# Performance work log

Hardware: AMD Instinct MI355X
Metric: run time of the kernel (lower is better)

Reference implementation:

```python
import jax, jax.numpy as jnp
import numpy as np

N = 200000
H = 128        # n_heads == input feature dim
HID = 512      # hidden_features
D_H = 512      # scaling denominator
C = 10.0       # tanh clip scale


def setup_inputs() -> dict:
    key = jax.random.key(0)
    k0, k1, k2, k3, k4, k5 = jax.random.split(key, 6)
    output = jax.random.normal(k0, (N, H), dtype=jnp.float32)
    # adjacency row: binary mask (which nodes are reachable neighbors)
    adj_modified = (jax.random.uniform(k1, (N,)) < 0.5).astype(jnp.float32)
    W1 = jax.random.normal(k2, (HID, H), dtype=jnp.float32) * (1.0 / np.sqrt(H))
    b1 = jax.random.normal(k3, (HID,), dtype=jnp.float32) * 0.01
    W2 = jax.random.normal(k4, (HID, H), dtype=jnp.float32) * (1.0 / np.sqrt(H))
    b2 = jax.random.normal(k5, (HID,), dtype=jnp.float32) * 0.01
    return {"output": output, "adj_modified": adj_modified,
            "W1": W1, "b1": b1, "W2": W2, "b2": b2, "prev_node": 5}


def reference(output, adj_modified, W1, b1, W2, b2, prev_node):
    # v_i: [1, H] embedding of the previously selected node
    v_i = output[prev_node][None, :]
    # v_j: [N, H] neighbor embeddings gated by the adjacency row
    v_j = adj_modified[:, None] * output
    phi1_v_i = v_i @ W1.T + b1          # [1, HID]
    phi2_v_j = v_j @ W2.T + b2          # [N, HID]
    scores = (phi1_v_i @ phi2_v_j.T) / jnp.sqrt(jnp.asarray(D_H, jnp.float32))  # [1, N]
    attn = C * jnp.tanh(scores) * adj_modified  # clipped + masked, [1, N]
    attn = attn[0]                                # [N]
    w = jax.nn.softmax(attn, axis=0)
    w = w * (attn != 0).astype(w.dtype)
    p = w.max()
    selected_node = jnp.argmax(w)
    return selected_node, p
```

## Files before the change

kernel.cpp:

```cpp
#include <hip/hip_runtime.h>
#include <math.h>

#define H 128
#define HID 512
#define GRID 2048
#define PREP_B 16

struct Ws {
    float sb_part[PREP_B];
    float u_part[PREP_B][H];
    unsigned long long best_part[GRID];
    float Z_part[GRID];
};

__device__ __forceinline__ unsigned int fkey(float f) {
    unsigned int u = __float_as_uint(f);
    return (u & 0x80000000u) ? ~u : (u | 0x80000000u);
}
__device__ __forceinline__ float inv_fkey(unsigned int k) {
    return __uint_as_float((k & 0x80000000u) ? (k ^ 0x80000000u) : ~k);
}

__global__ __launch_bounds__(256)
void prep_kernel(const float* __restrict__ outp, const float* __restrict__ W1,
                 const float* __restrict__ b1, const float* __restrict__ W2,
                 const float* __restrict__ b2, const int* __restrict__ prev,
                 Ws* __restrict__ ws) {
    __shared__ float phi1_s[32];
    __shared__ float sb_s[8];
    __shared__ float u_s[2][H];
    int t = threadIdx.x;
    int lane = t & 63;
    int c = lane & 31;
    int g = t >> 5;
    int kbase = blockIdx.x * 32;
    const float4* vi = (const float4*)(outp + (size_t)prev[0] * H);
    float4 v = vi[c];
    float sb = 0.f;
#pragma unroll
    for (int r = 0; r < 4; ++r) {
        int kl = g * 4 + r;
        int k = kbase + kl;
        float4 w = ((const float4*)(W1 + (size_t)k * H))[c];
        float d = w.x * v.x + w.y * v.y + w.z * v.z + w.w * v.w;
        d += __shfl_xor(d, 16);
        d += __shfl_xor(d, 8);
        d += __shfl_xor(d, 4);
        d += __shfl_xor(d, 2);
        d += __shfl_xor(d, 1);
        if (c == 0) {
            float phi = d + b1[k];
            phi1_s[kl] = phi;
            sb += phi * b2[k];
        }
    }
    if (c == 0) sb_s[g] = sb;
    __syncthreads();
    int h = t & 127;
    int g2 = t >> 7;
    float up = 0.f;
#pragma unroll
    for (int kk = 0; kk < 16; ++kk) {
        int kl = g2 * 16 + kk;
        up += phi1_s[kl] * W2[(size_t)(kbase + kl) * H + h];
    }
    u_s[g2][h] = up;
    __syncthreads();
    if (t < H) ws->u_part[blockIdx.x][t] = u_s[0][t] + u_s[1][t];
    if (t == 0) {
        float s = 0.f;
#pragma unroll
        for (int i = 0; i < 8; ++i) s += sb_s[i];
        ws->sb_part[blockIdx.x] = s;
    }
}

__global__ __launch_bounds__(256)
void score_kernel(const float4* __restrict__ xv, const float* __restrict__ adj,
                  Ws* __restrict__ ws, int n, int ntiles) {
    __shared__ float zs[4];
    __shared__ unsigned long long bs[4];
    const float inv = 0.04419417382415922f;
    int t = threadIdx.x;
    int lane = t & 63;
    int c = lane & 31;
    int hv = lane >> 5;
    int w = t >> 6;
    float4 uv = make_float4(0.f, 0.f, 0.f, 0.f);
    float s_b = 0.f;
#pragma unroll
    for (int b = 0; b < PREP_B; ++b) {
        float4 p = ((const float4*)ws->u_part[b])[c];
        uv.x += p.x; uv.y += p.y; uv.z += p.z; uv.w += p.w;
        s_b += ws->sb_part[b];
    }
    float zloc = 0.f;
    float bscore = -3.4e38f;
    int bidx = -1;
    for (int tile = blockIdx.x; tile < ntiles; tile += GRID) {
        int rowbase = tile * 32 + w * 8;
        float av = 0.f;
        if (lane < 8 && rowbase + lane < n) av = adj[rowbase + lane];
        float a4[4];
        float d[4];
#pragma unroll
        for (int r = 0; r < 4; ++r) {
            a4[r] = __shfl(av, hv + 2 * r);
            float dd = 0.f;
            if (a4[r] != 0.f) {
                int row = rowbase + hv + 2 * r;
                float4 x = xv[(size_t)row * 32 + c];
                dd = x.x * uv.x + x.y * uv.y + x.z * uv.z + x.w * uv.w;
            }
            d[r] = dd;
        }
#pragma unroll
        for (int r = 0; r < 4; ++r) {
            if (a4[r] != 0.f) {
                float dd = d[r];
                dd += __shfl_xor(dd, 16);
                dd += __shfl_xor(dd, 8);
                dd += __shfl_xor(dd, 4);
                dd += __shfl_xor(dd, 2);
                dd += __shfl_xor(dd, 1);
                d[r] = dd;
            }
        }
        if (c < 4) {
            int row = rowbase + hv + 2 * c;
            if (row < n) {
                float a = a4[0];
                float dm = d[0];
#pragma unroll
                for (int r = 1; r < 4; ++r) {
                    a  = (c == r) ? a4[r] : a;
                    dm = (c == r) ? d[r] : dm;
                }
                if (a != 0.f) {
                    float score = (s_b + a * dm) * inv;
                    float e = __expf(2.f * score);
                    float attn = 10.f * ((e - 1.f) / (e + 1.f));
                    zloc += __expf(attn);
                    if (score > bscore) { bscore = score; bidx = row; }
                } else {
                    zloc += 1.0f;
                }
            }
        }
    }
#pragma unroll
    for (int m = 32; m >= 1; m >>= 1) zloc += __shfl_xor(zloc, m);
    unsigned long long pk = 0ull;
    if (bidx >= 0)
        pk = ((unsigned long long)fkey(bscore) << 32) |
             (unsigned long long)(0xFFFFFFFFu - (unsigned int)bidx);
#pragma unroll
    for (int m = 32; m >= 1; m >>= 1) {
        unsigned long long o = __shfl_xor(pk, m);
        if (o > pk) pk = o;
    }
    if (lane == 0) { zs[w] = zloc; bs[w] = pk; }
    __syncthreads();
    if (t == 0) {
        float z = zs[0] + zs[1] + zs[2] + zs[3];
        unsigned long long p2 = bs[0];
#pragma unroll
        for (int i = 1; i < 4; ++i) if (bs[i] > p2) p2 = bs[i];
        ws->Z_part[blockIdx.x] = z;
        ws->best_part[blockIdx.x] = p2;
    }
}

__global__ __launch_bounds__(1024)
void reduce_kernel(const Ws* __restrict__ ws, float* __restrict__ outp) {
    __shared__ float zs[16];
    __shared__ unsigned long long bs[16];
    int t = threadIdx.x;
    int lane = t & 63;
    float z = ws->Z_part[t] + ws->Z_part[t + 1024];
    unsigned long long pk = ws->best_part[t];
    unsigned long long o2 = ws->best_part[t + 1024];
    if (o2 > pk) pk = o2;
#pragma unroll
    for (int m = 32; m >= 1; m >>= 1) {
        z += __shfl_xor(z, m);
        unsigned long long o = __shfl_xor(pk, m);
        if (o > pk) pk = o;
    }
    if (lane == 0) { zs[t >> 6] = z; bs[t >> 6] = pk; }
    __syncthreads();
    if (t == 0) {
        float Z = 0.f;
        unsigned long long b = 0ull;
#pragma unroll
        for (int i = 0; i < 16; ++i) { Z += zs[i]; if (bs[i] > b) b = bs[i]; }
        unsigned int idx = 0xFFFFFFFFu - (unsigned int)(b & 0xFFFFFFFFu);
        float score = inv_fkey((unsigned int)(b >> 32));
        float p = __expf(10.f * tanhf(score)) / Z;
        if (b == 0ull) { idx = 0; p = 0.f; }
        outp[0] = (float)idx;
        outp[1] = p;
    }
}

extern "C" void kernel_launch(void* const* d_in, const int* in_sizes, int n_in,
                              void* d_out, int out_size, void* d_ws, size_t ws_size,
                              hipStream_t stream) {
    const float* outp = (const float*)d_in[0];
    const float* adj  = (const float*)d_in[1];
    const float* W1   = (const float*)d_in[2];
    const float* b1   = (const float*)d_in[3];
    const float* W2   = (const float*)d_in[4];
    const float* b2   = (const float*)d_in[5];
    const int*   prev = (const int*)d_in[6];
    int n = in_sizes[1];
    Ws* ws = (Ws*)d_ws;

    int ntiles = (n + 31) / 32;

    prep_kernel<<<PREP_B, 256, 0, stream>>>(outp, W1, b1, W2, b2, prev, ws);
    score_kernel<<<GRID, 256, 0, stream>>>((const float4*)outp, adj, ws, n, ntiles);
    reduce_kernel<<<1, 1024, 0, stream>>>(ws, (float*)d_out);
}
```

Before: 167.4 us.

## Fuse final reduction into score kernel via last-block atomic counter and prefetch adj

```diff
diff --git a/kernel.cpp b/kernel.cpp
--- a/kernel.cpp
+++ b/kernel.cpp
@@ -11,6 +11,7 @@
     float u_part[PREP_B][H];
     unsigned long long best_part[GRID];
     float Z_part[GRID];
+    unsigned int done;
 };
 
 __device__ __forceinline__ unsigned int fkey(float f) {
@@ -30,6 +31,7 @@
     __shared__ float sb_s[8];
     __shared__ float u_s[2][H];
     int t = threadIdx.x;
+    if (blockIdx.x == 0 && t == 0) ws->done = 0u;
     int lane = t & 63;
     int c = lane & 31;
     int g = t >> 5;
@@ -77,9 +79,11 @@
 
 __global__ __launch_bounds__(256)
 void score_kernel(const float4* __restrict__ xv, const float* __restrict__ adj,
-                  Ws* __restrict__ ws, int n, int ntiles) {
+                  Ws* __restrict__ ws, float* __restrict__ outp,
+                  int n, int ntiles) {
     __shared__ float zs[4];
     __shared__ unsigned long long bs[4];
+    __shared__ int lastflag;
     const float inv = 0.04419417382415922f;
     int t = threadIdx.x;
     int lane = t & 63;
@@ -97,10 +101,21 @@
     float zloc = 0.f;
     float bscore = -3.4e38f;
     int bidx = -1;
-    for (int tile = blockIdx.x; tile < ntiles; tile += GRID) {
+
+    int tile = blockIdx.x;
+    float av = 0.f;
+    if (tile < ntiles) {
+        int rb = tile * 32 + w * 8;
+        if (lane < 8 && rb + lane < n) av = adj[rb + lane];
+    }
+    for (; tile < ntiles; tile += GRID) {
+        int tnext = tile + GRID;
+        float av_next = 0.f;
+        if (tnext < ntiles) {
+            int rbn = tnext * 32 + w * 8;
+            if (lane < 8 && rbn + lane < n) av_next = adj[rbn + lane];
+        }
         int rowbase = tile * 32 + w * 8;
-        float av = 0.f;
-        if (lane < 8 && rowbase + lane < n) av = adj[rowbase + lane];
         float a4[4];
         float d[4];
 #pragma unroll
@@ -147,6 +162,7 @@
                 }
             }
         }
+        av = av_next;
     }
 #pragma unroll
     for (int m = 32; m >= 1; m >>= 1) zloc += __shfl_xor(zloc, m);
@@ -166,34 +182,41 @@
         unsigned long long p2 = bs[0];
 #pragma unroll
         for (int i = 1; i < 4; ++i) if (bs[i] > p2) p2 = bs[i];
-        ws->Z_part[blockIdx.x] = z;
-        ws->best_part[blockIdx.x] = p2;
-    }
-}
-
-__global__ __launch_bounds__(1024)
-void reduce_kernel(const Ws* __restrict__ ws, float* __restrict__ outp) {
-    __shared__ float zs[16];
-    __shared__ unsigned long long bs[16];
-    int t = threadIdx.x;
-    int lane = t & 63;
-    float z = ws->Z_part[t] + ws->Z_part[t + 1024];
-    unsigned long long pk = ws->best_part[t];
-    unsigned long long o2 = ws->best_part[t + 1024];
-    if (o2 > pk) pk = o2;
+        __hip_atomic_store(&ws->Z_part[blockIdx.x], z,
+                           __ATOMIC_RELAXED, __HIP_MEMORY_SCOPE_AGENT);
+        __hip_atomic_store(&ws->best_part[blockIdx.x], p2,
+                           __ATOMIC_RELAXED, __HIP_MEMORY_SCOPE_AGENT);
+        unsigned int prevc = __hip_atomic_fetch_add(&ws->done, 1u,
+                           __ATOMIC_ACQ_REL, __HIP_MEMORY_SCOPE_AGENT);
+        lastflag = (prevc == GRID - 1) ? 1 : 0;
+    }
+    __syncthreads();
+    if (!lastflag) return;
+
+    float z = 0.f;
+    unsigned long long pk2 = 0ull;
+#pragma unroll
+    for (int i = 0; i < GRID / 256; ++i) {
+        int s = t + i * 256;
+        z += __hip_atomic_load(&ws->Z_part[s],
+                               __ATOMIC_RELAXED, __HIP_MEMORY_SCOPE_AGENT);
+        unsigned long long o = __hip_atomic_load(&ws->best_part[s],
+                               __ATOMIC_RELAXED, __HIP_MEMORY_SCOPE_AGENT);
+        if (o > pk2) pk2 = o;
+    }
 #pragma unroll
     for (int m = 32; m >= 1; m >>= 1) {
         z += __shfl_xor(z, m);
-        unsigned long long o = __shfl_xor(pk, m);
-        if (o > pk) pk = o;
-    }
-    if (lane == 0) { zs[t >> 6] = z; bs[t >> 6] = pk; }
+        unsigned long long o = __shfl_xor(pk2, m);
+        if (o > pk2) pk2 = o;
+    }
+    if (lane == 0) { zs[w] = z; bs[w] = pk2; }
     __syncthreads();
     if (t == 0) {
-        float Z = 0.f;
-        unsigned long long b = 0ull;
-#pragma unroll
-        for (int i = 0; i < 16; ++i) { Z += zs[i]; if (bs[i] > b) b = bs[i]; }
+        float Z = zs[0] + zs[1] + zs[2] + zs[3];
+        unsigned long long b = bs[0];
+#pragma unroll
+        for (int i = 1; i < 4; ++i) if (bs[i] > b) b = bs[i];
         unsigned int idx = 0xFFFFFFFFu - (unsigned int)(b & 0xFFFFFFFFu);
         float score = inv_fkey((unsigned int)(b >> 32));
         float p = __expf(10.f * tanhf(score)) / Z;
@@ -219,6 +242,6 @@
     int ntiles = (n + 31) / 32;
 
     prep_kernel<<<PREP_B, 256, 0, stream>>>(outp, W1, b1, W2, b2, prev, ws);
-    score_kernel<<<GRID, 256, 0, stream>>>((const float4*)outp, adj, ws, n, ntiles);
-    reduce_kernel<<<1, 1024, 0, stream>>>(ws, (float*)d_out);
-}
+    score_kernel<<<GRID, 256, 0, stream>>>((const float4*)outp, adj, ws,
+                                           (float*)d_out, n, ntiles);
+}
```

Result: slower. 223.6 us (+33.6%).
